# Kernel optimization log

Hardware: AMD Instinct MI355X
Metric: run time of the kernel (lower is better)

The kernel has to match this reference:

```python
import jax, jax.numpy as jnp
import numpy as np

K = 5000  # module's self.dim

def setup_inputs() -> dict:
    key = jax.random.key(0)
    x = jax.random.normal(key, (50_000_000,), dtype=jnp.float32)
    return {"x": x}

def reference(x):
    # top-k values and their indices (lax.top_k returns them sorted by value,
    # but the subsequent argsort over indices restores original-index order,
    # matching torch.topk(sorted=False) + argsort + gather exactly)
    vals, idx = jax.lax.top_k(x, K)          # [K], [K]
    order = jnp.argsort(idx)                 # permutation restoring input order
    return vals[order]                       # [K] order-preserving top-k subset
```

## Files before the change

kernel.cpp:

```cpp
#include <hip/hip_runtime.h>

#define K_TOP 5000
#define NBIN 2048
#define CAND_LDS 1024
#define NB_BUCKET 4096
#define TARGET_SAMPLED 94u

__device__ __forceinline__ unsigned f2key(float f) {
    unsigned u = __float_as_uint(f);
    return (u & 0x80000000u) ? ~u : (u | 0x80000000u);
}
__device__ __forceinline__ float key2f(unsigned k) {
    unsigned u = (k & 0x80000000u) ? (k ^ 0x80000000u) : ~k;
    return __uint_as_float(u);
}

__global__ __launch_bounds__(256) void k_sample(const float4* __restrict__ x4, long n4,
                                                unsigned* __restrict__ hist) {
    __shared__ unsigned lh[NBIN];
    for (int i = threadIdx.x; i < NBIN; i += 256) lh[i] = 0;
    __syncthreads();
    int wave = threadIdx.x >> 6;
    int lane = threadIdx.x & 63;
    long gw = (long)blockIdx.x * 4 + wave;
    long totW = (long)gridDim.x * 4;
    long nChunk = (n4 + 8191) / 8192;
    for (long c = gw; c < nChunk; c += totW) {
        long i = c * 8192 + lane;
        if (i < n4) {
            float4 v = x4[i];
            atomicAdd(&lh[f2key(v.x) >> 21], 1u);
            atomicAdd(&lh[f2key(v.y) >> 21], 1u);
            atomicAdd(&lh[f2key(v.z) >> 21], 1u);
            atomicAdd(&lh[f2key(v.w) >> 21], 1u);
        }
    }
    __syncthreads();
    for (int i = threadIdx.x; i < NBIN; i += 256) {
        unsigned c = lh[i];
        if (c) atomicAdd(&hist[i], c);
    }
}

__global__ __launch_bounds__(256) void k_findbin(const unsigned* __restrict__ hist,
                                                 unsigned* __restrict__ ctrl) {
    __shared__ unsigned lh[NBIN];
    __shared__ unsigned gs[64];
    for (int i = threadIdx.x; i < NBIN; i += 256) lh[i] = hist[i];
    __syncthreads();
    int t = threadIdx.x;
    if (t < 64) {
        unsigned s = 0;
        for (int j = 0; j < 32; j++) s += lh[t * 32 + j];
        gs[t] = s;
    }
    __syncthreads();
    if (t == 0) {
        unsigned cum = 0;
        int g = 63;
        for (; g > 0; g--) { if (cum + gs[g] >= TARGET_SAMPLED) break; cum += gs[g]; }
        int b = g * 32 + 31;
        for (; b > g * 32; b--) { if (cum + lh[b] >= TARGET_SAMPLED) break; cum += lh[b]; }
        ctrl[1] = ((unsigned)b) << 21;
    }
}

__global__ __launch_bounds__(256) void k_compact(const float4* __restrict__ x4, long n4,
                                                 long n, const float* __restrict__ x,
                                                 unsigned* __restrict__ ctrl,
                                                 unsigned* __restrict__ candKey,
                                                 unsigned* __restrict__ candIdx,
                                                 unsigned capC) {
    __shared__ unsigned sKey[CAND_LDS], sIdx[CAND_LDS];
    __shared__ unsigned sCnt, sBase;
    if (threadIdx.x == 0) sCnt = 0;
    __syncthreads();
    unsigned L = ctrl[1];
    unsigned* candCount = &ctrl[0];

    int tail = (int)(n & 3);
    if (blockIdx.x == 0 && threadIdx.x < tail) {
        unsigned k = f2key(x[n4 * 4 + threadIdx.x]);
        if (k >= L) {
            unsigned p = atomicAdd(&sCnt, 1u);
            if (p < CAND_LDS) { sKey[p] = k; sIdx[p] = (unsigned)(n4 * 4 + threadIdx.x); }
            else {
                unsigned q = atomicAdd(candCount, 1u);
                if (q < capC) { candKey[q] = k; candIdx[q] = (unsigned)(n4 * 4 + threadIdx.x); }
            }
        }
    }

    long tiles = (n4 + 1023) >> 10;
    for (long tile = blockIdx.x; tile < tiles; tile += gridDim.x) {
        long base = tile << 10;
        long i0 = base + threadIdx.x;
        long i1 = i0 + 256, i2 = i0 + 512, i3 = i0 + 768;
        bool in0 = i0 < n4, in1 = i1 < n4, in2 = i2 < n4, in3 = i3 < n4;
        float4 v0, v1, v2, v3;
        if (in0) v0 = x4[i0];
        if (in1) v1 = x4[i1];
        if (in2) v2 = x4[i2];
        if (in3) v3 = x4[i3];
#define PROC(vv, inb, ii)                                                            \
        if (inb) {                                                                   \
            unsigned kk, bb = (unsigned)((ii) * 4);                                  \
            kk = f2key((vv).x);                                                      \
            if (kk >= L) { unsigned p = atomicAdd(&sCnt, 1u);                        \
                if (p < CAND_LDS) { sKey[p] = kk; sIdx[p] = bb; }                    \
                else { unsigned q = atomicAdd(candCount, 1u);                        \
                       if (q < capC) { candKey[q] = kk; candIdx[q] = bb; } } }       \
            kk = f2key((vv).y);                                                      \
            if (kk >= L) { unsigned p = atomicAdd(&sCnt, 1u);                        \
                if (p < CAND_LDS) { sKey[p] = kk; sIdx[p] = bb + 1; }                \
                else { unsigned q = atomicAdd(candCount, 1u);                        \
                       if (q < capC) { candKey[q] = kk; candIdx[q] = bb + 1; } } }   \
            kk = f2key((vv).z);                                                      \
            if (kk >= L) { unsigned p = atomicAdd(&sCnt, 1u);                        \
                if (p < CAND_LDS) { sKey[p] = kk; sIdx[p] = bb + 2; }                \
                else { unsigned q = atomicAdd(candCount, 1u);                        \
                       if (q < capC) { candKey[q] = kk; candIdx[q] = bb + 2; } } }   \
            kk = f2key((vv).w);                                                      \
            if (kk >= L) { unsigned p = atomicAdd(&sCnt, 1u);                        \
                if (p < CAND_LDS) { sKey[p] = kk; sIdx[p] = bb + 3; }                \
                else { unsigned q = atomicAdd(candCount, 1u);                        \
                       if (q < capC) { candKey[q] = kk; candIdx[q] = bb + 3; } } }   \
        }
        PROC(v0, in0, i0)
        PROC(v1, in1, i1)
        PROC(v2, in2, i2)
        PROC(v3, in3, i3)
#undef PROC
    }
    __syncthreads();
    unsigned cnt = sCnt; if (cnt > CAND_LDS) cnt = CAND_LDS;
    if (threadIdx.x == 0) sBase = atomicAdd(candCount, cnt);
    __syncthreads();
    unsigned bp = sBase;
    for (unsigned i = threadIdx.x; i < cnt; i += 256) {
        unsigned q = bp + i;
        if (q < capC) { candKey[q] = sKey[i]; candIdx[q] = sIdx[i]; }
    }
}

__global__ __launch_bounds__(1024) void k_final(const unsigned* __restrict__ candKey,
                                                const unsigned* __restrict__ candIdx,
                                                unsigned* __restrict__ ctrl, unsigned capC,
                                                unsigned* __restrict__ selKey,
                                                unsigned* __restrict__ selIdx,
                                                unsigned* __restrict__ selKeyS,
                                                unsigned* __restrict__ selIdxS,
                                                float* __restrict__ out, long n, int bshift) {
    __shared__ unsigned h[NB_BUCKET * 2];
    __shared__ unsigned part[1024];
    __shared__ unsigned part2[32];
    __shared__ unsigned res[2];
    __shared__ unsigned sScalar;
    const int t = threadIdx.x;
    unsigned Nc = ctrl[0]; if (Nc > capC) Nc = capC;
    unsigned L = ctrl[1];

    unsigned mk = 0;
    for (unsigned i = t; i < Nc; i += 1024) { unsigned k = candKey[i]; if (k > mk) mk = k; }
    part[t] = mk;
    __syncthreads();
    if (t < 32) { unsigned m = 0; for (int j = 0; j < 32; j++) { unsigned v = part[t * 32 + j]; if (v > m) m = v; } part2[t] = m; }
    __syncthreads();
    if (t == 0) { unsigned m = 0; for (int j = 0; j < 32; j++) if (part2[j] > m) m = part2[j]; sScalar = m; }
    __syncthreads();
    unsigned maxK = sScalar;

    unsigned lo = L, target = K_TOP;
    unsigned range = maxK - lo;
    int shift = 0;
    while ((range >> shift) >= NBIN) shift++;
    for (;;) {
        int nb = (int)(range >> shift) + 1;
        for (int i = t; i < nb; i += 1024) h[i] = 0;
        __syncthreads();
        for (unsigned i = t; i < Nc; i += 1024) {
            unsigned d = candKey[i] - lo;
            if (d <= range) atomicAdd(&h[d >> shift], 1u);
        }
        __syncthreads();
        int ng = (nb + 31) >> 5;
        if (t < ng) {
            unsigned s = 0; int b0 = t * 32, e = b0 + 32; if (e > nb) e = nb;
            for (int j = b0; j < e; j++) s += h[j];
            part[t] = s;
        }
        __syncthreads();
        if (t == 0) {
            unsigned cum = 0; int g = ng - 1;
            for (; g > 0; g--) { if (cum + part[g] >= target) break; cum += part[g]; }
            int hi2 = g * 32 + 31; if (hi2 > nb - 1) hi2 = nb - 1;
            int b = hi2;
            for (; b > g * 32; b--) { if (cum + h[b] >= target) break; cum += h[b]; }
            res[0] = (unsigned)b; res[1] = target - cum;
        }
        __syncthreads();
        lo += res[0] << shift; target = res[1];
        if (shift == 0) break;
        range = (1u << shift) - 1;
        shift = (shift > 11) ? shift - 11 : 0;
    }
    unsigned T = lo, R = target;

    if (t == 0) sScalar = 0;
    __syncthreads();
    for (unsigned i = t; i < Nc; i += 1024)
        if (candKey[i] == T) atomicAdd(&sScalar, 1u);
    __syncthreads();
    unsigned cntEq = sScalar;
    unsigned idxCut = 0xFFFFFFFFu;
    if (cntEq != R) {
        unsigned lo2 = 0, tgt = R;
        unsigned range2 = (unsigned)(n - 1);
        int sh = 0;
        while ((range2 >> sh) >= NBIN) sh++;
        for (;;) {
            int nb = (int)(range2 >> sh) + 1;
            for (int i = t; i < nb; i += 1024) h[i] = 0;
            __syncthreads();
            for (unsigned i = t; i < Nc; i += 1024)
                if (candKey[i] == T) {
                    unsigned d = candIdx[i] - lo2;
                    if (d <= range2) atomicAdd(&h[d >> sh], 1u);
                }
            __syncthreads();
            int ng = (nb + 31) >> 5;
            if (t < ng) {
                unsigned s = 0; int b0 = t * 32, e = b0 + 32; if (e > nb) e = nb;
                for (int j = b0; j < e; j++) s += h[j];
                part[t] = s;
            }
            __syncthreads();
            if (t == 0) {
                unsigned cum = 0; int g = 0;
                for (; g < ng - 1; g++) { if (cum + part[g] >= tgt) break; cum += part[g]; }
                int b = g * 32; int hi2 = g * 32 + 31; if (hi2 > nb - 1) hi2 = nb - 1;
                for (; b < hi2; b++) { if (cum + h[b] >= tgt) break; cum += h[b]; }
                res[0] = (unsigned)b; res[1] = tgt - cum;
            }
            __syncthreads();
            lo2 += res[0] << sh; tgt = res[1];
            if (sh == 0) break;
            range2 = (1u << sh) - 1;
            sh = (sh > 11) ? sh - 11 : 0;
        }
        idxCut = lo2;
    }
    __syncthreads();

    for (int i = t; i < NB_BUCKET; i += 1024) h[i] = 0;
    if (t == 0) sScalar = 0;
    __syncthreads();
    for (unsigned i = t; i < Nc; i += 1024) {
        unsigned k = candKey[i]; unsigned id = candIdx[i];
        if (k > T || (k == T && id <= idxCut)) {
            unsigned p = atomicAdd(&sScalar, 1u);
            if (p < K_TOP) {
                selKey[p] = k; selIdx[p] = id;
                atomicAdd(&h[id >> bshift], 1u);
            }
        }
    }
    __syncthreads();
    unsigned nSel = sScalar; if (nSel > K_TOP) nSel = K_TOP;

    unsigned* bc = h;
    unsigned* bs = h + NB_BUCKET;
    { unsigned s = 0; for (int j = 0; j < 4; j++) s += bc[t * 4 + j]; part[t] = s; }
    __syncthreads();
    if (t < 32) { unsigned s = 0; for (int j = 0; j < 32; j++) s += part[t * 32 + j]; part2[t] = s; }
    __syncthreads();
    if (t == 0) { unsigned run = 0; for (int j = 0; j < 32; j++) { unsigned v = part2[j]; part2[j] = run; run += v; } }
    __syncthreads();
    if (t < 32) { unsigned run = part2[t]; for (int j = 0; j < 32; j++) { int id2 = t * 32 + j; unsigned v = part[id2]; part[id2] = run; run += v; } }
    __syncthreads();
    { unsigned run = part[t]; for (int j = 0; j < 4; j++) { bs[t * 4 + j] = run; run += bc[t * 4 + j]; } }
    __syncthreads();

    for (unsigned g = t; g < nSel; g += 1024) {
        unsigned id = selIdx[g];
        unsigned b = id >> bshift;
        unsigned p = atomicAdd(&bs[b], 1u);
        if (p < K_TOP) { selKeyS[p] = selKey[g]; selIdxS[p] = id; }
    }
    __syncthreads();

    for (int j = 0; j < 4; j++) {
        int b = t * 4 + j;
        unsigned cnt = bc[b];
        if (!cnt) continue;
        unsigned s = bs[b] - cnt;
        for (unsigned i = 0; i < cnt; i++) {
            unsigned mi = i, mv = selIdxS[s + i];
            for (unsigned q = i + 1; q < cnt; q++) {
                unsigned v = selIdxS[s + q];
                if (v < mv) { mv = v; mi = q; }
            }
            if (mi != i) {
                unsigned ti = selIdxS[s + i]; selIdxS[s + i] = selIdxS[s + mi]; selIdxS[s + mi] = ti;
                unsigned tk = selKeyS[s + i]; selKeyS[s + i] = selKeyS[s + mi]; selKeyS[s + mi] = tk;
            }
            out[s + i] = key2f(selKeyS[s + i]);
        }
    }
}

extern "C" void kernel_launch(void* const* d_in, const int* in_sizes, int n_in,
                              void* d_out, int out_size, void* d_ws, size_t ws_size,
                              hipStream_t stream) {
    const float* x = (const float*)d_in[0];
    long n = in_sizes[0];
    float* out = (float*)d_out;
    unsigned* w = (unsigned*)d_ws;

    unsigned* hist    = w;
    unsigned* ctrl    = w + 2048;
    unsigned* selKey  = w + 2056;
    unsigned* selIdx  = w + 7056;
    unsigned* selKeyS = w + 12056;
    unsigned* selIdxS = w + 17056;
    const size_t CAND_BASE = 24576;
    size_t words = ws_size / 4;
    unsigned capC = 0;
    if (words > CAND_BASE + 64) {
        size_t c = (words - CAND_BASE) / 2;
        if (c > (size_t)(4u << 20)) c = (size_t)(4u << 20);
        capC = (unsigned)c;
    }
    unsigned* candKey = w + CAND_BASE;
    unsigned* candIdx = candKey + capC;

    int bshift = 0;
    while (((n - 1) >> bshift) >= NB_BUCKET) bshift++;

    hipMemsetAsync(d_ws, 0, 2056u * 4u + 32u, stream);

    long n4 = n / 4;
    k_sample<<<256, 256, 0, stream>>>((const float4*)x, n4, hist);
    k_findbin<<<1, 256, 0, stream>>>(hist, ctrl);
    k_compact<<<4096, 256, 0, stream>>>((const float4*)x, n4, n, x, ctrl,
                                        candKey, candIdx, capC);
    k_final<<<1, 1024, 0, stream>>>(candKey, candIdx, ctrl, capC,
                                    selKey, selIdx, selKeyS, selIdxS, out, n, bshift);
}
```

Measured before the change: 369.5 us.

## Fuse findbin into sample via last-block pattern, widen compact tiles, ballot-aggregate selection

The threshold-bin search is folded into the sampling kernel: a completion counter in ctrl[4] lets the last finishing block read the global histogram and pick the bin, which removes one kernel launch. The compaction kernel now loads 8 float4 per thread per tile instead of 4 and launches half as many blocks, giving more memory loads in flight per thread. In the final kernel, the equal-key count becomes a reduction through shared memory instead of per-element LDS atomics, and selection uses wave-level ballot/popcount so each wave issues one atomic. The risks are higher register pressure in compaction and reliance on the ctrl[4] counter being zeroed by the existing memset each call.

```diff
diff --git a/kernel.cpp b/kernel.cpp
--- a/kernel.cpp
+++ b/kernel.cpp
@@ -16,8 +16,11 @@
 }
 
 __global__ __launch_bounds__(256) void k_sample(const float4* __restrict__ x4, long n4,
-                                                unsigned* __restrict__ hist) {
+                                                unsigned* __restrict__ hist,
+                                                unsigned* __restrict__ ctrl) {
     __shared__ unsigned lh[NBIN];
+    __shared__ unsigned gs[64];
+    __shared__ unsigned lastFlag;
     for (int i = threadIdx.x; i < NBIN; i += 256) lh[i] = 0;
     __syncthreads();
     int wave = threadIdx.x >> 6;
@@ -40,13 +43,14 @@
         unsigned c = lh[i];
         if (c) atomicAdd(&hist[i], c);
     }
-}
-
-__global__ __launch_bounds__(256) void k_findbin(const unsigned* __restrict__ hist,
-                                                 unsigned* __restrict__ ctrl) {
-    __shared__ unsigned lh[NBIN];
-    __shared__ unsigned gs[64];
-    for (int i = threadIdx.x; i < NBIN; i += 256) lh[i] = hist[i];
+    __threadfence();
+    if (threadIdx.x == 0)
+        lastFlag = (atomicAdd(&ctrl[4], 1u) == gridDim.x - 1) ? 1u : 0u;
+    __syncthreads();
+    if (!lastFlag) return;
+    __threadfence();
+    for (int i = threadIdx.x; i < NBIN; i += 256)
+        lh[i] = __hip_atomic_load(&hist[i], __ATOMIC_RELAXED, __HIP_MEMORY_SCOPE_AGENT);
     __syncthreads();
     int t = threadIdx.x;
     if (t < 64) {
@@ -91,17 +95,6 @@
         }
     }
 
-    long tiles = (n4 + 1023) >> 10;
-    for (long tile = blockIdx.x; tile < tiles; tile += gridDim.x) {
-        long base = tile << 10;
-        long i0 = base + threadIdx.x;
-        long i1 = i0 + 256, i2 = i0 + 512, i3 = i0 + 768;
-        bool in0 = i0 < n4, in1 = i1 < n4, in2 = i2 < n4, in3 = i3 < n4;
-        float4 v0, v1, v2, v3;
-        if (in0) v0 = x4[i0];
-        if (in1) v1 = x4[i1];
-        if (in2) v2 = x4[i2];
-        if (in3) v3 = x4[i3];
 #define PROC(vv, inb, ii)                                                            \
         if (inb) {                                                                   \
             unsigned kk, bb = (unsigned)((ii) * 4);                                  \
@@ -126,12 +119,26 @@
                 else { unsigned q = atomicAdd(candCount, 1u);                        \
                        if (q < capC) { candKey[q] = kk; candIdx[q] = bb + 3; } } }   \
         }
-        PROC(v0, in0, i0)
-        PROC(v1, in1, i1)
-        PROC(v2, in2, i2)
-        PROC(v3, in3, i3)
+
+    long tiles = (n4 + 2047) >> 11;
+    for (long tile = blockIdx.x; tile < tiles; tile += gridDim.x) {
+        long base = tile << 11;
+        long i0 = base + threadIdx.x;
+        float4 v[8];
+        long  ii[8];
+        bool  in[8];
+        #pragma unroll
+        for (int j = 0; j < 8; j++) {
+            ii[j] = i0 + (long)j * 256;
+            in[j] = ii[j] < n4;
+            if (in[j]) v[j] = x4[ii[j]];
+        }
+        #pragma unroll
+        for (int j = 0; j < 8; j++) {
+            PROC(v[j], in[j], ii[j])
+        }
+    }
 #undef PROC
-    }
     __syncthreads();
     unsigned cnt = sCnt; if (cnt > CAND_LDS) cnt = CAND_LDS;
     if (threadIdx.x == 0) sBase = atomicAdd(candCount, cnt);
@@ -157,6 +164,7 @@
     __shared__ unsigned res[2];
     __shared__ unsigned sScalar;
     const int t = threadIdx.x;
+    const int lane = t & 63;
     unsigned Nc = ctrl[0]; if (Nc > capC) Nc = capC;
     unsigned L = ctrl[1];
 
@@ -206,11 +214,16 @@
     }
     unsigned T = lo, R = target;
 
-    if (t == 0) sScalar = 0;
-    __syncthreads();
-    for (unsigned i = t; i < Nc; i += 1024)
-        if (candKey[i] == T) atomicAdd(&sScalar, 1u);
-    __syncthreads();
+    {
+        unsigned loc = 0;
+        for (unsigned i = t; i < Nc; i += 1024) loc += (candKey[i] == T) ? 1u : 0u;
+        part[t] = loc;
+        __syncthreads();
+        if (t < 32) { unsigned s = 0; for (int j = 0; j < 32; j++) s += part[t * 32 + j]; part2[t] = s; }
+        __syncthreads();
+        if (t == 0) { unsigned s = 0; for (int j = 0; j < 32; j++) s += part2[j]; sScalar = s; }
+        __syncthreads();
+    }
     unsigned cntEq = sScalar;
     unsigned idxCut = 0xFFFFFFFFu;
     if (cntEq != R) {
@@ -257,11 +270,19 @@
     __syncthreads();
     for (unsigned i = t; i < Nc; i += 1024) {
         unsigned k = candKey[i]; unsigned id = candIdx[i];
-        if (k > T || (k == T && id <= idxCut)) {
-            unsigned p = atomicAdd(&sScalar, 1u);
-            if (p < K_TOP) {
-                selKey[p] = k; selIdx[p] = id;
-                atomicAdd(&h[id >> bshift], 1u);
+        bool sel = (k > T) || (k == T && id <= idxCut);
+        unsigned long long m = __ballot(sel);
+        if (m) {
+            int leader = (int)__ffsll((unsigned long long)m) - 1;
+            unsigned base = 0;
+            if (lane == leader) base = atomicAdd(&sScalar, (unsigned)__popcll(m));
+            base = __shfl(base, leader);
+            if (sel) {
+                unsigned p = base + (unsigned)__popcll(m & ((1ull << lane) - 1ull));
+                if (p < K_TOP) {
+                    selKey[p] = k; selIdx[p] = id;
+                    atomicAdd(&h[id >> bshift], 1u);
+                }
             }
         }
     }
@@ -340,9 +361,8 @@
     hipMemsetAsync(d_ws, 0, 2056u * 4u + 32u, stream);
 
     long n4 = n / 4;
-    k_sample<<<256, 256, 0, stream>>>((const float4*)x, n4, hist);
-    k_findbin<<<1, 256, 0, stream>>>(hist, ctrl);
-    k_compact<<<4096, 256, 0, stream>>>((const float4*)x, n4, n, x, ctrl,
+    k_sample<<<256, 256, 0, stream>>>((const float4*)x, n4, hist, ctrl);
+    k_compact<<<2048, 256, 0, stream>>>((const float4*)x, n4, n, x, ctrl,
                                         candKey, candIdx, capC);
     k_final<<<1, 1024, 0, stream>>>(candKey, candIdx, ctrl, capC,
                                     selKey, selIdx, selKeyS, selIdxS, out, n, bshift);
```

After: 375.5 us. No clear change (+1.6%).
